# Optimization experiments

Measured on AMD Instinct MI355X. Metric: run time of the kernel, lower is better.

The kernel has to match this reference:

```python
import jax, jax.numpy as jnp
import numpy as np

EPS = 1e-5
CHUNK = 256
N_LAYERS = 4
D_MODEL = 1024
D_INNER = 2048
D_HEAD = 64
N_HEADS = 32
D_STATE = 64
D_CONV = 4
CONV_DIM = D_INNER + 2 * D_STATE  # ngroups=1
D_IN_PROJ = 2 * D_INNER + 2 * D_STATE + N_HEADS


def silu(x):
    return x * jax.nn.sigmoid(x)


def rmsnorm(x, w):
    return x * jax.lax.rsqrt(jnp.mean(x * x, axis=-1, keepdims=True) + EPS) * w


def segsum(x):
    # x: [..., T] -> [..., T, T] lower-triangular segment sums, -inf above diag
    T = x.shape[-1]
    cs = jnp.cumsum(x, axis=-1)
    ss = cs[..., :, None] - cs[..., None, :]
    mask = jnp.tril(jnp.ones((T, T), dtype=bool))
    return jnp.where(mask, ss, -jnp.inf)


def ssd(X, A, B, C, chunk):
    # X: [b,l,h,p] (already scaled by dt), A: [b,l,h] (= dt * A_head), B,C: [b,l,n] (ngroups=1)
    b, l, h, p = X.shape
    c = l // chunk
    X = X.reshape(b, c, chunk, h, p)
    A = A.reshape(b, c, chunk, h).transpose(0, 3, 1, 2)  # [b,h,c,l]
    B = B.reshape(b, c, chunk, -1)
    C = C.reshape(b, c, chunk, -1)
    Acs = jnp.cumsum(A, axis=-1)  # [b,h,c,l]
    # intra-chunk (diagonal blocks)
    Lm = jnp.exp(segsum(A))  # [b,h,c,l,l]
    Y_diag = jnp.einsum('bcln,bcsn,bhcls,bcshp->bclhp', C, B, Lm, X)
    # chunk end states
    decay_states = jnp.exp(Acs[..., -1:] - Acs)  # [b,h,c,l]
    states = jnp.einsum('bcln,bhcl,bclhp->bchpn', B, decay_states, X)
    # inter-chunk recurrence (c is small -> dense segsum over chunks)
    A_last = jnp.pad(Acs[..., -1], ((0, 0), (0, 0), (1, 0)))  # [b,h,c+1]
    decay_chunk = jnp.exp(segsum(A_last))  # [b,h,c+1,c+1]
    states = jnp.concatenate([jnp.zeros_like(states[:, :1]), states], axis=1)
    new_states = jnp.einsum('bhzc,bchpn->bzhpn', decay_chunk, states)
    states = new_states[:, :-1]  # state entering each chunk
    Y_off = jnp.einsum('bcln,bchpn,bhcl->bclhp', C, states, jnp.exp(Acs))
    return (Y_diag + Y_off).reshape(b, l, h, p)


def mamba2_layer(x, in_w, conv_w, conv_b, dt_bias, A_log, D, gnorm_w, out_w):
    b, l, _ = x.shape
    zxbcdt = jnp.einsum('bld,ed->ble', x, in_w)  # [b,l,D_IN_PROJ]
    z = zxbcdt[..., :D_INNER]
    xBC = zxbcdt[..., D_INNER:D_INNER + CONV_DIM]
    dt = zxbcdt[..., D_INNER + CONV_DIM:]  # [b,l,h]
    # depthwise causal conv1d + silu
    xpad = jnp.pad(xBC, ((0, 0), (D_CONV - 1, 0), (0, 0)))
    xconv = conv_b
    for k in range(D_CONV):
        xconv = xconv + xpad[:, k:k + l, :] * conv_w[:, k]
    xBC = silu(xconv)
    x_in = xBC[..., :D_INNER]
    B = xBC[..., D_INNER:D_INNER + D_STATE]
    C = xBC[..., D_INNER + D_STATE:]
    dt = jax.nn.softplus(dt + dt_bias)  # [b,l,h]
    A = -jnp.exp(A_log)  # [h]
    X = x_in.reshape(b, l, N_HEADS, D_HEAD)
    y = ssd(X * dt[..., None], dt * A, B, C, CHUNK)
    y = y + D[None, None, :, None] * X
    y = y.reshape(b, l, D_INNER)
    y = rmsnorm(y * silu(z), gnorm_w)
    return jnp.einsum('ble,de->bld', y, out_w)


def setup_inputs() -> dict:
    key = jax.random.key(0)
    ks = jax.random.split(key, 8)
    x = jax.random.normal(ks[0], (2, 2048, D_MODEL), dtype=jnp.float32)
    in_proj_w = jax.random.normal(ks[1], (N_LAYERS, D_IN_PROJ, D_MODEL), dtype=jnp.float32) * 0.02
    conv_w = jax.random.uniform(ks[2], (N_LAYERS, CONV_DIM, D_CONV), dtype=jnp.float32, minval=-0.5, maxval=0.5)
    conv_b = jnp.zeros((N_LAYERS, CONV_DIM), dtype=jnp.float32)
    A_log = jnp.log(jax.random.uniform(ks[3], (N_LAYERS, N_HEADS), dtype=jnp.float32, minval=1.0, maxval=16.0))
    dt0 = jax.random.uniform(ks[4], (N_LAYERS, N_HEADS), dtype=jnp.float32, minval=0.001, maxval=0.1)
    dt_bias = dt0 + jnp.log(-jnp.expm1(-dt0))  # inverse softplus
    D = jnp.ones((N_LAYERS, N_HEADS), dtype=jnp.float32)
    gnorm_w = jnp.ones((N_LAYERS, D_INNER), dtype=jnp.float32)
    out_proj_w = jax.random.normal(ks[5], (N_LAYERS, D_MODEL, D_INNER), dtype=jnp.float32) * 0.02
    rms_w = jnp.ones((N_LAYERS, D_MODEL), dtype=jnp.float32)
    return {"x": x, "in_proj_w": in_proj_w, "conv_w": conv_w, "conv_b": conv_b,
            "dt_bias": dt_bias, "A_log": A_log, "D": D, "gnorm_w": gnorm_w,
            "out_proj_w": out_proj_w, "rms_w": rms_w}


def reference(x, in_proj_w, conv_w, conv_b, dt_bias, A_log, D, gnorm_w, out_proj_w, rms_w):
    for i in range(N_LAYERS):
        x = x + mamba2_layer(rmsnorm(x, rms_w[i]), in_proj_w[i], conv_w[i], conv_b[i],
                             dt_bias[i], A_log[i], D[i], gnorm_w[i], out_proj_w[i])
    return x
```

## Files before the change

kernel.cpp:

```cpp
#include <hip/hip_runtime.h>
#include <cmath>

#define BATCH 2
#define LSEQ 2048
#define DMODEL 1024
#define DINNER 2048
#define NHEADS 32
#define DHEAD 64
#define DSTATE 64
#define DCONV 4
#define CONVDIM (DINNER + 2*DSTATE)
#define DINPROJ (2*DINNER + 2*DSTATE + NHEADS)
#define DINPROJ_PAD 4352
#define CHUNKSZ 256
#define NCHUNK (LSEQ/CHUNKSZ)
#define MROWS (BATCH*LSEQ)
#define EPSF 1e-5f

typedef __attribute__((ext_vector_type(8))) short shortx8;
typedef __attribute__((ext_vector_type(4))) short shortx4;
typedef __attribute__((ext_vector_type(4))) float floatx4;

__device__ __forceinline__ ushort f2bf(float f) {
  unsigned u = __float_as_uint(f);
  unsigned r = (u + 0x7fffu + ((u >> 16) & 1u)) >> 16;
  return (ushort)r;
}
__device__ __forceinline__ float bf2f(ushort b) {
  return __uint_as_float(((unsigned)b) << 16);
}

__device__ __forceinline__ shortx8 pack8(float4 a, float4 b) {
  shortx8 r;
  r[0] = (short)f2bf(a.x); r[1] = (short)f2bf(a.y);
  r[2] = (short)f2bf(a.z); r[3] = (short)f2bf(a.w);
  r[4] = (short)f2bf(b.x); r[5] = (short)f2bf(b.y);
  r[6] = (short)f2bf(b.z); r[7] = (short)f2bf(b.w);
  return r;
}

__device__ __forceinline__ void async_load16(const void* g, void* l) {
  __builtin_amdgcn_global_load_lds(
      (const __attribute__((address_space(1))) void*)g,
      (__attribute__((address_space(3))) void*)l, 16, 0, 0);
}

__device__ __forceinline__ float block_reduce_sum_256(float v, float* sb) {
  for (int off = 32; off > 0; off >>= 1) v += __shfl_down(v, off, 64);
  int lane = threadIdx.x & 63, wid = threadIdx.x >> 6;
  if (lane == 0) sb[wid] = v;
  __syncthreads();
  return sb[0] + sb[1] + sb[2] + sb[3];
}

__global__ __launch_bounds__(256) void cvt_bf16_k(const float* __restrict__ src,
                                                  ushort* __restrict__ dst,
                                                  size_t n_src, size_t n_dst) {
  size_t i = (size_t)blockIdx.x * 256 + threadIdx.x;
  if (i >= n_dst) return;
  float v = (i < n_src) ? src[i] : 0.f;
  dst[i] = f2bf(v);
}

__global__ __launch_bounds__(256) void rmsnorm_k(const float* __restrict__ x,
                                                 const float* __restrict__ w,
                                                 ushort* __restrict__ out) {
  __shared__ float sb[4];
  int r = blockIdx.x;
  const float* xr = x + (size_t)r * DMODEL;
  ushort* orow = out + (size_t)r * DMODEL;
  float v[4]; float ssq = 0.f;
  for (int i = 0; i < 4; i++) {
    v[i] = xr[threadIdx.x + i * 256];
    ssq += v[i] * v[i];
  }
  float s = block_reduce_sum_256(ssq, sb);
  float sc = rsqrtf(s / (float)DMODEL + EPSF);
  for (int i = 0; i < 4; i++) {
    int c = threadIdx.x + i * 256;
    orow[c] = f2bf(v[i] * sc * w[c]);
  }
}

__device__ __forceinline__ void stage_tile(const ushort* __restrict__ A,
                                           const ushort* __restrict__ B,
                                           char* lb, int m0, int n0, int K, int k0,
                                           int wid, int rA, int sA) {
#pragma unroll
  for (int rd = 0; rd < 2; rd++) {
    int r = rd * 64 + rA;
    int sl = sA ^ ((r ^ (r >> 2)) & 3);
    async_load16(A + (size_t)(m0 + r) * K + (k0 + sl * 8), lb + rd * 4096 + wid * 1024);
  }
#pragma unroll
  for (int rd = 0; rd < 2; rd++) {
    int r = rd * 64 + rA;
    int sl = sA ^ ((r ^ (r >> 2)) & 3);
    async_load16(B + (size_t)(n0 + r) * K + (k0 + sl * 8), lb + 8192 + rd * 4096 + wid * 1024);
  }
}

__global__ __launch_bounds__(256, 2) void gemm_nt_mfma_pipe(const ushort* __restrict__ A,
                                                            const ushort* __restrict__ B,
                                                            float* __restrict__ C,
                                                            ushort* __restrict__ Cbf,
                                                            const float* __restrict__ resid,
                                                            int M, int N, int K) {
  __shared__ __align__(16) char lds[4][16384];
  int tid = threadIdx.x;
  int wid = tid >> 6, lane = tid & 63;
  int quad = lane >> 4, lrow = lane & 15;
  int m0 = blockIdx.y * 128, n0 = blockIdx.x * 128;
  int wm = (wid >> 1) * 64, wn = (wid & 1) * 64;
  int rA = tid >> 2, sA = tid & 3;

  floatx4 acc[4][4];
#pragma unroll
  for (int i = 0; i < 4; i++)
#pragma unroll
    for (int j = 0; j < 4; j++) acc[i][j] = (floatx4){0.f, 0.f, 0.f, 0.f};

  int NT = K >> 5;
#pragma unroll
  for (int t = 0; t < 3; t++)
    if (t < NT) stage_tile(A, B, lds[t & 3], m0, n0, K, t * 32, wid, rA, sA);

  for (int t = 0; t < NT; t++) {
    if (t + 3 < NT) stage_tile(A, B, lds[(t + 3) & 3], m0, n0, K, (t + 3) * 32, wid, rA, sA);
    int rem = NT - 1 - t;
    if (rem >= 3)      asm volatile("s_waitcnt vmcnt(12)" ::: "memory");
    else if (rem == 2) asm volatile("s_waitcnt vmcnt(8)" ::: "memory");
    else if (rem == 1) asm volatile("s_waitcnt vmcnt(4)" ::: "memory");
    else               asm volatile("s_waitcnt vmcnt(0)" ::: "memory");
    __builtin_amdgcn_s_barrier();
    __builtin_amdgcn_sched_barrier(0);

    const char* Ab = lds[t & 3];
    const char* Bb = Ab + 8192;
    shortx8 af[4], bfr[4];
#pragma unroll
    for (int i = 0; i < 4; i++) {
      int r = wm + i * 16 + lrow;
      af[i] = *(const shortx8*)(Ab + r * 64 + ((quad ^ ((r ^ (r >> 2)) & 3)) << 4));
    }
#pragma unroll
    for (int j = 0; j < 4; j++) {
      int r = wn + j * 16 + lrow;
      bfr[j] = *(const shortx8*)(Bb + r * 64 + ((quad ^ ((r ^ (r >> 2)) & 3)) << 4));
    }
    __builtin_amdgcn_s_setprio(1);
#pragma unroll
    for (int i = 0; i < 4; i++)
#pragma unroll
      for (int j = 0; j < 4; j++)
        acc[i][j] = __builtin_amdgcn_mfma_f32_16x16x32_bf16(af[i], bfr[j], acc[i][j], 0, 0, 0);
    __builtin_amdgcn_s_setprio(0);
    __builtin_amdgcn_sched_barrier(0);
    __builtin_amdgcn_s_barrier();
    __builtin_amdgcn_sched_barrier(0);
  }

  if (Cbf) {
#pragma unroll
    for (int i = 0; i < 4; i++) {
      int r0 = m0 + wm + i * 16 + quad * 4;
#pragma unroll
      for (int j = 0; j < 4; j++) {
        int n = n0 + wn + j * 16 + lrow;
        if (n < N)
#pragma unroll
          for (int r = 0; r < 4; r++)
            Cbf[(size_t)(r0 + r) * N + n] = f2bf(acc[i][j][r]);
      }
    }
  } else {
    bool hasR = (resid != nullptr);
#pragma unroll
    for (int i = 0; i < 4; i++) {
      int r0 = m0 + wm + i * 16 + quad * 4;
#pragma unroll
      for (int j = 0; j < 4; j++) {
        int n = n0 + wn + j * 16 + lrow;
        if (n < N) {
#pragma unroll
          for (int r = 0; r < 4; r++) {
            size_t idx = (size_t)(r0 + r) * N + n;
            float v = acc[i][j][r];
            if (hasR) v += resid[idx];
            C[idx] = v;
          }
        }
      }
    }
  }
}

__global__ __launch_bounds__(256) void conv_silu_k(const ushort* __restrict__ zxbf,
                                                   const float* __restrict__ cw,
                                                   const float* __restrict__ cb,
                                                   ushort* __restrict__ xbf) {
  int ch = blockIdx.x * 256 + threadIdx.x;
  if (ch >= CONVDIM) return;
  int r = blockIdx.y;
  int b = r >> 11, l = r & (LSEQ - 1);
  float acc = cb[ch];
  for (int k = 0; k < DCONV; k++) {
    int ls = l - (DCONV - 1) + k;
    if (ls >= 0)
      acc += bf2f(zxbf[(size_t)(b * LSEQ + ls) * DINPROJ + DINNER + ch]) * cw[ch * DCONV + k];
  }
  float s = acc / (1.f + expf(-acc));
  xbf[(size_t)r * CONVDIM + ch] = f2bf(s);
}

__global__ __launch_bounds__(256) void cumsum_k(const ushort* __restrict__ zxbf,
                                                const float* __restrict__ dt_bias,
                                                const float* __restrict__ A_log,
                                                float* __restrict__ dt_sp,
                                                float* __restrict__ dtA_cs) {
  __shared__ float buf[256];
  int bid = blockIdx.x;
  int h = bid & 31, c = (bid >> 5) & 7, b = bid >> 8;
  int l = threadIdx.x;
  float Aneg = -expf(A_log[h]);
  int row = b * LSEQ + c * CHUNKSZ + l;
  float v = bf2f(zxbf[(size_t)row * DINPROJ + DINNER + CONVDIM + h]) + dt_bias[h];
  float dtv = (v > 20.f) ? v : log1pf(expf(v));
  dt_sp[row * 32 + h] = dtv;
  buf[l] = dtv * Aneg;
  __syncthreads();
  for (int off = 1; off < 256; off <<= 1) {
    float add = (l >= off) ? buf[l - off] : 0.f;
    __syncthreads();
    buf[l] += add;
    __syncthreads();
  }
  dtA_cs[(size_t)bid * CHUNKSZ + l] = buf[l];
}

#define ST_STRIDE 72
__global__ __launch_bounds__(256) void states_mfma(const ushort* __restrict__ xbf,
                                                   const float* __restrict__ dt_sp,
                                                   const float* __restrict__ dtA_cs,
                                                   float* __restrict__ st_raw) {
  __shared__ ushort XT[64 * ST_STRIDE];
  __shared__ ushort BT[64 * ST_STRIDE];
  __shared__ float wrow[64];
  int bid = blockIdx.x;
  int h = bid & 31, c = (bid >> 5) & 7, b = bid >> 8;
  int tid = threadIdx.x;
  int w = tid >> 6, lane = tid & 63;
  int quad = lane >> 4, lrow = lane & 15;
  int cbase = bid * CHUNKSZ;
  int rowbase = b * LSEQ + c * CHUNKSZ;
  float T = dtA_cs[cbase + CHUNKSZ - 1];
  floatx4 acc[4];
  for (int jt = 0; jt < 4; jt++) acc[jt] = (floatx4){0.f, 0.f, 0.f, 0.f};
  int half = tid & 31, srb = tid >> 5;
  for (int lt = 0; lt < 4; lt++) {
    __syncthreads();
    if (tid < 64) {
      int row = rowbase + lt * 64 + tid;
      wrow[tid] = dt_sp[row * 32 + h] * __expf(T - dtA_cs[cbase + lt * 64 + tid]);
    }
    __syncthreads();
    for (int pass = 0; pass < 8; pass++) {
      int sr = srb + pass * 8;
      int row = rowbase + lt * 64 + sr;
      uint bv = *(const uint*)(xbf + (size_t)row * CONVDIM + DINNER + 2 * half);
      uint xv = *(const uint*)(xbf + (size_t)row * CONVDIM + h * DHEAD + 2 * half);
      float wv = wrow[sr];
      BT[(2 * half) * ST_STRIDE + sr]     = (ushort)(bv & 0xffff);
      BT[(2 * half + 1) * ST_STRIDE + sr] = (ushort)(bv >> 16);
      XT[(2 * half) * ST_STRIDE + sr]     = f2bf(bf2f((ushort)(xv & 0xffff)) * wv);
      XT[(2 * half + 1) * ST_STRIDE + sr] = f2bf(bf2f((ushort)(xv >> 16)) * wv);
    }
    __syncthreads();
    for (int kk = 0; kk < 64; kk += 32) {
      shortx8 af = *(const shortx8*)&XT[(w * 16 + lrow) * ST_STRIDE + kk + quad * 8];
      for (int jt = 0; jt < 4; jt++) {
        shortx8 bf = *(const shortx8*)&BT[(jt * 16 + lrow) * ST_STRIDE + kk + quad * 8];
        acc[jt] = __builtin_amdgcn_mfma_f32_16x16x32_bf16(af, bf, acc[jt], 0, 0, 0);
      }
    }
  }
  size_t base = (size_t)bid * (DHEAD * DSTATE);
  for (int jt = 0; jt < 4; jt++) {
    int n = jt * 16 + lrow;
    for (int r = 0; r < 4; r++) {
      int p = w * 16 + quad * 4 + r;
      st_raw[base + (size_t)p * 64 + n] = acc[jt][r];
    }
  }
}

__global__ __launch_bounds__(256) void scan_k(float* __restrict__ st,
                                              const float* __restrict__ dtA_cs) {
  int bid = blockIdx.x;
  int h = bid & 31, b = bid >> 5;
  int tid = threadIdx.x;
  float s[16];
  for (int i = 0; i < 16; i++) s[i] = 0.f;
  for (int c = 0; c < NCHUNK; c++) {
    int g = (b * NCHUNK + c) * 32 + h;
    float dec = expf(dtA_cs[(size_t)g * CHUNKSZ + CHUNKSZ - 1]);
    size_t base = (size_t)g * (DHEAD * DSTATE);
    for (int i = 0; i < 16; i++) {
      int idx = tid + i * 256;
      float raw = st[base + idx];
      st[base + idx] = s[i];
      s[i] = s[i] * dec + raw;
    }
  }
}

#define BS_STRIDE 72
#define XT_STRIDE 68
#define PW_STRIDE 72
__global__ __launch_bounds__(256) void ydiag_mfma(const ushort* __restrict__ xbf,
                                                  const float* __restrict__ dt_sp,
                                                  const float* __restrict__ dtA_cs,
                                                  const float* __restrict__ st_in,
                                                  ushort* __restrict__ Y) {
  __shared__ ushort Bs[64 * BS_STRIDE];
  __shared__ ushort XsT[64 * XT_STRIDE];
  __shared__ ushort Pw[4 * 16 * PW_STRIDE];
  __shared__ float cs[256];
  int tid = threadIdx.x;
  int w = tid >> 6, lane = tid & 63;
  int quad = lane >> 4, lrow = lane & 15;
  int bid = blockIdx.x;
  int lt = bid & 3, h = (bid >> 2) & 31, c = (bid >> 7) & 7, b = bid >> 10;
  int g = (b * NCHUNK + c) * 32 + h;
  int cbase = g * CHUNKSZ;
  int rowbase = b * LSEQ + c * CHUNKSZ;

  cs[tid] = dtA_cs[cbase + tid];
  __syncthreads();

  int mrow = lt * 64 + w * 16;
  float csl[4];
  for (int r = 0; r < 4; r++) csl[r] = cs[mrow + quad * 4 + r];

  shortx8 Cf[2];
  {
    const ushort* cp = xbf + (size_t)(rowbase + mrow + lrow) * CONVDIM + DINNER + DSTATE;
    for (int q = 0; q < 2; q++)
      Cf[q] = *(const shortx8*)(cp + q * 32 + quad * 8);
  }

  floatx4 acc[4];
  for (int jt = 0; jt < 4; jt++) acc[jt] = (floatx4){0.f, 0.f, 0.f, 0.f};
  const float* stp = st_in + (size_t)g * (DHEAD * DSTATE);
  for (int q = 0; q < 2; q++) {
    for (int jt = 0; jt < 4; jt++) {
      const float* sp = stp + (size_t)(jt * 16 + lrow) * 64 + q * 32 + quad * 8;
      shortx8 sf = pack8(*(const float4*)sp, *(const float4*)(sp + 4));
      acc[jt] = __builtin_amdgcn_mfma_f32_16x16x32_bf16(Cf[q], sf, acc[jt], 0, 0, 0);
    }
  }
  for (int jt = 0; jt < 4; jt++)
    for (int r = 0; r < 4; r++) acc[jt][r] *= __expf(csl[r]);

  ushort* myP = Pw + w * 16 * PW_STRIDE;
  int half = tid & 31, srb = tid >> 5;
  for (int st = 0; st <= lt; st++) {
    __syncthreads();
    for (int pass = 0; pass < 8; pass++) {
      int sr = srb + pass * 8;
      int row = rowbase + st * 64 + sr;
      uint bv = *(const uint*)(xbf + (size_t)row * CONVDIM + DINNER + 2 * half);
      *(uint*)&Bs[sr * BS_STRIDE + 2 * half] = bv;
      float dtv = dt_sp[row * 32 + h];
      uint xv = *(const uint*)(xbf + (size_t)row * CONVDIM + h * DHEAD + 2 * half);
      XsT[(2 * half) * XT_STRIDE + sr]     = f2bf(bf2f((ushort)(xv & 0xffff)) * dtv);
      XsT[(2 * half + 1) * XT_STRIDE + sr] = f2bf(bf2f((ushort)(xv >> 16)) * dtv);
    }
    __syncthreads();
    for (int jt = 0; jt < 4; jt++) {
      floatx4 s = (floatx4){0.f, 0.f, 0.f, 0.f};
      for (int q = 0; q < 2; q++) {
        shortx8 bfr = *(const shortx8*)&Bs[(jt * 16 + lrow) * BS_STRIDE + q * 32 + quad * 8];
        s = __builtin_amdgcn_mfma_f32_16x16x32_bf16(Cf[q], bfr, s, 0, 0, 0);
      }
      int scol = st * 64 + jt * 16 + lrow;
      float css = cs[scol];
      for (int r = 0; r < 4; r++) {
        int l = mrow + quad * 4 + r;
        float v = (scol <= l) ? s[r] * __expf(csl[r] - css) : 0.f;
        myP[(quad * 4 + r) * PW_STRIDE + jt * 16 + lrow] = f2bf(v);
      }
    }
    shortx8 pf[2];
    for (int q = 0; q < 2; q++)
      pf[q] = *(const shortx8*)&myP[lrow * PW_STRIDE + q * 32 + quad * 8];
    for (int jt = 0; jt < 4; jt++) {
      for (int q = 0; q < 2; q++) {
        const ushort* xp = &XsT[(jt * 16 + lrow) * XT_STRIDE + q * 32 + quad * 8];
        shortx4 lo = *(const shortx4*)xp;
        shortx4 hi = *(const shortx4*)(xp + 4);
        shortx8 xf = __builtin_shufflevector(lo, hi, 0, 1, 2, 3, 4, 5, 6, 7);
        acc[jt] = __builtin_amdgcn_mfma_f32_16x16x32_bf16(pf[q], xf, acc[jt], 0, 0, 0);
      }
    }
  }
  int growb = rowbase + mrow + quad * 4;
  for (int jt = 0; jt < 4; jt++)
    for (int r = 0; r < 4; r++)
      Y[(size_t)(growb + r) * DINNER + h * DHEAD + jt * 16 + lrow] = f2bf(acc[jt][r]);
}

__global__ __launch_bounds__(256) void gatenorm_k(const ushort* __restrict__ Ybf,
                                                  const ushort* __restrict__ zxbf,
                                                  const ushort* __restrict__ xbf,
                                                  const float* __restrict__ Dvec,
                                                  const float* __restrict__ gw,
                                                  ushort* __restrict__ obf) {
  __shared__ float sb[4];
  int r = blockIdx.x;
  const ushort* yr = Ybf + (size_t)r * DINNER;
  const ushort* zr = zxbf + (size_t)r * DINPROJ;
  const ushort* xr = xbf + (size_t)r * CONVDIM;
  ushort* orow = obf + (size_t)r * DINNER;
  float t[8]; float ssq = 0.f;
  for (int i = 0; i < 8; i++) {
    int cc = threadIdx.x + i * 256;
    float z = bf2f(zr[cc]);
    float yv = bf2f(yr[cc]) + Dvec[cc >> 6] * bf2f(xr[cc]);
    float gv = yv * (z / (1.f + expf(-z)));
    t[i] = gv;
    ssq += gv * gv;
  }
  float s = block_reduce_sum_256(ssq, sb);
  float sc = rsqrtf(s / (float)DINNER + EPSF);
  for (int i = 0; i < 8; i++) {
    int cc = threadIdx.x + i * 256;
    orow[cc] = f2bf(t[i] * sc * gw[cc]);
  }
}

extern "C" void kernel_launch(void* const* d_in, const int* in_sizes, int n_in,
                              void* d_out, int out_size, void* d_ws, size_t ws_size,
                              hipStream_t stream) {
  const float* x_in     = (const float*)d_in[0];
  const float* in_w     = (const float*)d_in[1];
  const float* conv_w   = (const float*)d_in[2];
  const float* conv_b   = (const float*)d_in[3];
  const float* dt_bias  = (const float*)d_in[4];
  const float* A_log    = (const float*)d_in[5];
  const float* Dvec     = (const float*)d_in[6];
  const float* gnorm_w  = (const float*)d_in[7];
  const float* out_w    = (const float*)d_in[8];
  const float* rms_w    = (const float*)d_in[9];
  float* out = (float*)d_out;

  float* ws = (float*)d_ws;
  size_t o = 0;
  float* x_cur  = ws + o; o += (size_t)MROWS * DMODEL;
  ushort* zx_bf = (ushort*)(ws + o); o += (size_t)MROWS * DINPROJ / 2;
  ushort* xbf   = (ushort*)(ws + o); o += (size_t)MROWS * CONVDIM / 2;
  float* dt_sp  = ws + o; o += (size_t)MROWS * NHEADS;
  float* dtA_cs = ws + o; o += (size_t)BATCH * NCHUNK * NHEADS * CHUNKSZ;
  float* st     = ws + o; o += (size_t)BATCH * NCHUNK * NHEADS * DHEAD * DSTATE;
  ushort* Ybf   = (ushort*)(ws + o); o += (size_t)MROWS * DINNER / 2;
  ushort* act_bf = (ushort*)(ws + o); o += (size_t)MROWS * DINNER / 2;
  ushort* w_bf   = (ushort*)(ws + o); o += (size_t)DINPROJ_PAD * DMODEL / 2;

  hipMemcpyAsync(x_cur, x_in, (size_t)MROWS * DMODEL * sizeof(float),
                 hipMemcpyDeviceToDevice, stream);

  for (int i = 0; i < 4; i++) {
    const float* in_w_i   = in_w    + (size_t)i * DINPROJ * DMODEL;
    const float* conv_w_i = conv_w  + (size_t)i * CONVDIM * DCONV;
    const float* conv_b_i = conv_b  + (size_t)i * CONVDIM;
    const float* dtb_i    = dt_bias + (size_t)i * NHEADS;
    const float* Alog_i   = A_log   + (size_t)i * NHEADS;
    const float* D_i      = Dvec    + (size_t)i * NHEADS;
    const float* gw_i     = gnorm_w + (size_t)i * DINNER;
    const float* out_w_i  = out_w   + (size_t)i * DMODEL * DINNER;
    const float* rms_w_i  = rms_w   + (size_t)i * DMODEL;

    {
      size_t ns = (size_t)DINPROJ * DMODEL, nd = (size_t)DINPROJ_PAD * DMODEL;
      cvt_bf16_k<<<(nd + 255) / 256, 256, 0, stream>>>(in_w_i, w_bf, ns, nd);
    }
    rmsnorm_k<<<MROWS, 256, 0, stream>>>(x_cur, rms_w_i, act_bf);
    gemm_nt_mfma_pipe<<<dim3(DINPROJ_PAD / 128, MROWS / 128), 256, 0, stream>>>(
        act_bf, w_bf, nullptr, zx_bf, nullptr, MROWS, DINPROJ, DMODEL);
    conv_silu_k<<<dim3((CONVDIM + 255) / 256, MROWS), 256, 0, stream>>>(
        zx_bf, conv_w_i, conv_b_i, xbf);
    cumsum_k<<<BATCH * NCHUNK * NHEADS, 256, 0, stream>>>(zx_bf, dtb_i, Alog_i, dt_sp, dtA_cs);
    states_mfma<<<BATCH * NCHUNK * NHEADS, 256, 0, stream>>>(xbf, dt_sp, dtA_cs, st);
    scan_k<<<BATCH * NHEADS, 256, 0, stream>>>(st, dtA_cs);
    ydiag_mfma<<<BATCH * NCHUNK * NHEADS * 4, 256, 0, stream>>>(
        xbf, dt_sp, dtA_cs, st, Ybf);
    gatenorm_k<<<MROWS, 256, 0, stream>>>(Ybf, zx_bf, xbf, D_i, gw_i, act_bf);
    {
      size_t ns = (size_t)DMODEL * DINNER;
      cvt_bf16_k<<<(ns + 255) / 256, 256, 0, stream>>>(out_w_i, w_bf, ns, ns);
    }
    float* outC = (i == 3) ? out : x_cur;
    gemm_nt_mfma_pipe<<<dim3(DMODEL / 128, MROWS / 128), 256, 0, stream>>>(
        act_bf, w_bf, outC, nullptr, x_cur, MROWS, DMODEL, DINNER);
  }
}
```

Measured before the change: 1.085 ms.

## Remap GEMM blocks per XCD, five-buffer pipeline, vectorize conv, split scan

The GEMM now uses a 1D grid and remaps block IDs so that each of the 8 XCDs works on a contiguous rectangle of output tiles, which should improve L2 reuse. It also moves from a 4-slot to a 5-slot LDS ring, letting it drop the trailing barrier in each k-iteration. The depthwise conv is rewritten so each thread computes 8 channels by 8 rows from a vectorized sliding window. The state scan is split across 4 blocks per head to raise parallelism. The extra LDS (80KB per block) may reduce occupancy below the declared 2 blocks per CU.

New measurement: 988.0 us. -9.0%, faster.

```diff
diff --git a/kernel.cpp b/kernel.cpp
--- a/kernel.cpp
+++ b/kernel.cpp
@@ -105,12 +105,21 @@
                                                             float* __restrict__ C,
                                                             ushort* __restrict__ Cbf,
                                                             const float* __restrict__ resid,
-                                                            int M, int N, int K) {
-  __shared__ __align__(16) char lds[4][16384];
+                                                            int M, int N, int K,
+                                                            int nbx, int rw, int rh) {
+  __shared__ __align__(16) char lds[5][16384];
   int tid = threadIdx.x;
   int wid = tid >> 6, lane = tid & 63;
   int quad = lane >> 4, lrow = lane & 15;
-  int m0 = blockIdx.y * 128, n0 = blockIdx.x * 128;
+
+  int d = blockIdx.x;
+  int xcd = d & 7, wi = d >> 3;
+  int ra = nbx / rw;
+  int rn = xcd % ra, rm = xcd / ra;
+  int bx = rn * rw + wi % rw;
+  int by = rm * rh + wi / rw;
+
+  int m0 = by * 128, n0 = bx * 128;
   int wm = (wid >> 1) * 64, wn = (wid & 1) * 64;
   int rA = tid >> 2, sA = tid & 3;
 
@@ -123,10 +132,15 @@
   int NT = K >> 5;
 #pragma unroll
   for (int t = 0; t < 3; t++)
-    if (t < NT) stage_tile(A, B, lds[t & 3], m0, n0, K, t * 32, wid, rA, sA);
-
+    stage_tile(A, B, lds[t], m0, n0, K, t * 32, wid, rA, sA);
+
+  int cur = 0, sb = 3;
   for (int t = 0; t < NT; t++) {
-    if (t + 3 < NT) stage_tile(A, B, lds[(t + 3) & 3], m0, n0, K, (t + 3) * 32, wid, rA, sA);
+    __builtin_amdgcn_sched_barrier(0);
+    if (t + 3 < NT) {
+      stage_tile(A, B, lds[sb], m0, n0, K, (t + 3) * 32, wid, rA, sA);
+      sb = (sb == 4) ? 0 : sb + 1;
+    }
     int rem = NT - 1 - t;
     if (rem >= 3)      asm volatile("s_waitcnt vmcnt(12)" ::: "memory");
     else if (rem == 2) asm volatile("s_waitcnt vmcnt(8)" ::: "memory");
@@ -135,8 +149,9 @@
     __builtin_amdgcn_s_barrier();
     __builtin_amdgcn_sched_barrier(0);
 
-    const char* Ab = lds[t & 3];
+    const char* Ab = lds[cur];
     const char* Bb = Ab + 8192;
+    cur = (cur == 4) ? 0 : cur + 1;
     shortx8 af[4], bfr[4];
 #pragma unroll
     for (int i = 0; i < 4; i++) {
@@ -155,9 +170,6 @@
       for (int j = 0; j < 4; j++)
         acc[i][j] = __builtin_amdgcn_mfma_f32_16x16x32_bf16(af[i], bfr[j], acc[i][j], 0, 0, 0);
     __builtin_amdgcn_s_setprio(0);
-    __builtin_amdgcn_sched_barrier(0);
-    __builtin_amdgcn_s_barrier();
-    __builtin_amdgcn_sched_barrier(0);
   }
 
   if (Cbf) {
@@ -195,22 +207,52 @@
   }
 }
 
-__global__ __launch_bounds__(256) void conv_silu_k(const ushort* __restrict__ zxbf,
-                                                   const float* __restrict__ cw,
-                                                   const float* __restrict__ cb,
-                                                   ushort* __restrict__ xbf) {
-  int ch = blockIdx.x * 256 + threadIdx.x;
-  if (ch >= CONVDIM) return;
-  int r = blockIdx.y;
-  int b = r >> 11, l = r & (LSEQ - 1);
-  float acc = cb[ch];
-  for (int k = 0; k < DCONV; k++) {
-    int ls = l - (DCONV - 1) + k;
-    if (ls >= 0)
-      acc += bf2f(zxbf[(size_t)(b * LSEQ + ls) * DINPROJ + DINNER + ch]) * cw[ch * DCONV + k];
-  }
-  float s = acc / (1.f + expf(-acc));
-  xbf[(size_t)r * CONVDIM + ch] = f2bf(s);
+__global__ __launch_bounds__(256) void conv_silu_v2(const ushort* __restrict__ zxbf,
+                                                    const float* __restrict__ cw,
+                                                    const float* __restrict__ cb,
+                                                    ushort* __restrict__ xbf) {
+  int r0 = blockIdx.x * 8;
+  int bstart = r0 & ~(LSEQ - 1);
+  int tid = threadIdx.x;
+#pragma unroll
+  for (int rep = 0; rep < 2; rep++) {
+    int ch;
+    if (rep == 0) ch = tid * 8;
+    else { if (tid >= (CONVDIM - 2048) / 8) break; ch = 2048 + tid * 8; }
+    float wv[8][4], bias[8];
+#pragma unroll
+    for (int j = 0; j < 8; j++) {
+      float4 w4 = *(const float4*)(cw + (ch + j) * 4);
+      wv[j][0] = w4.x; wv[j][1] = w4.y; wv[j][2] = w4.z; wv[j][3] = w4.w;
+      bias[j] = cb[ch + j];
+    }
+    float xw[11][8];
+#pragma unroll
+    for (int wr = 0; wr < 11; wr++) {
+      int rr = r0 - 3 + wr;
+      if (rr < bstart) {
+#pragma unroll
+        for (int j = 0; j < 8; j++) xw[wr][j] = 0.f;
+      } else {
+        shortx8 v = *(const shortx8*)(zxbf + (size_t)rr * DINPROJ + DINNER + ch);
+#pragma unroll
+        for (int j = 0; j < 8; j++) xw[wr][j] = bf2f((ushort)v[j]);
+      }
+    }
+#pragma unroll
+    for (int o = 0; o < 8; o++) {
+      shortx8 ov;
+#pragma unroll
+      for (int j = 0; j < 8; j++) {
+        float acc = bias[j];
+#pragma unroll
+        for (int k = 0; k < 4; k++) acc += xw[o + k][j] * wv[j][k];
+        float s = acc / (1.f + expf(-acc));
+        ov[j] = (short)f2bf(s);
+      }
+      *(shortx8*)(xbf + (size_t)(r0 + o) * CONVDIM + ch) = ov;
+    }
+  }
 }
 
 __global__ __launch_bounds__(256) void cumsum_k(const ushort* __restrict__ zxbf,
@@ -297,15 +339,16 @@
 __global__ __launch_bounds__(256) void scan_k(float* __restrict__ st,
                                               const float* __restrict__ dtA_cs) {
   int bid = blockIdx.x;
-  int h = bid & 31, b = bid >> 5;
+  int seg = bid & 3, h = (bid >> 2) & 31, b = bid >> 7;
   int tid = threadIdx.x;
-  float s[16];
-  for (int i = 0; i < 16; i++) s[i] = 0.f;
+  int off = seg * 1024;
+  float s[4];
+  for (int i = 0; i < 4; i++) s[i] = 0.f;
   for (int c = 0; c < NCHUNK; c++) {
     int g = (b * NCHUNK + c) * 32 + h;
     float dec = expf(dtA_cs[(size_t)g * CHUNKSZ + CHUNKSZ - 1]);
-    size_t base = (size_t)g * (DHEAD * DSTATE);
-    for (int i = 0; i < 16; i++) {
+    size_t base = (size_t)g * (DHEAD * DSTATE) + off;
+    for (int i = 0; i < 4; i++) {
       int idx = tid + i * 256;
       float raw = st[base + idx];
       st[base + idx] = s[i];
@@ -485,13 +528,13 @@
       cvt_bf16_k<<<(nd + 255) / 256, 256, 0, stream>>>(in_w_i, w_bf, ns, nd);
     }
     rmsnorm_k<<<MROWS, 256, 0, stream>>>(x_cur, rms_w_i, act_bf);
-    gemm_nt_mfma_pipe<<<dim3(DINPROJ_PAD / 128, MROWS / 128), 256, 0, stream>>>(
-        act_bf, w_bf, nullptr, zx_bf, nullptr, MROWS, DINPROJ, DMODEL);
-    conv_silu_k<<<dim3((CONVDIM + 255) / 256, MROWS), 256, 0, stream>>>(
-        zx_bf, conv_w_i, conv_b_i, xbf);
+    gemm_nt_mfma_pipe<<<(DINPROJ_PAD / 128) * (MROWS / 128), 256, 0, stream>>>(
+        act_bf, w_bf, nullptr, zx_bf, nullptr, MROWS, DINPROJ, DMODEL,
+        DINPROJ_PAD / 128, 17, 8);
+    conv_silu_v2<<<MROWS / 8, 256, 0, stream>>>(zx_bf, conv_w_i, conv_b_i, xbf);
     cumsum_k<<<BATCH * NCHUNK * NHEADS, 256, 0, stream>>>(zx_bf, dtb_i, Alog_i, dt_sp, dtA_cs);
     states_mfma<<<BATCH * NCHUNK * NHEADS, 256, 0, stream>>>(xbf, dt_sp, dtA_cs, st);
-    scan_k<<<BATCH * NHEADS, 256, 0, stream>>>(st, dtA_cs);
+    scan_k<<<BATCH * NHEADS * 4, 256, 0, stream>>>(st, dtA_cs);
     ydiag_mfma<<<BATCH * NCHUNK * NHEADS * 4, 256, 0, stream>>>(
         xbf, dt_sp, dtA_cs, st, Ybf);
     gatenorm_k<<<MROWS, 256, 0, stream>>>(Ybf, zx_bf, xbf, D_i, gw_i, act_bf);
@@ -500,7 +543,8 @@
       cvt_bf16_k<<<(ns + 255) / 256, 256, 0, stream>>>(out_w_i, w_bf, ns, ns);
     }
     float* outC = (i == 3) ? out : x_cur;
-    gemm_nt_mfma_pipe<<<dim3(DMODEL / 128, MROWS / 128), 256, 0, stream>>>(
-        act_bf, w_bf, outC, nullptr, x_cur, MROWS, DMODEL, DINNER);
-  }
-}
+    gemm_nt_mfma_pipe<<<(DMODEL / 128) * (MROWS / 128), 256, 0, stream>>>(
+        act_bf, w_bf, outC, nullptr, x_cur, MROWS, DMODEL, DINNER,
+        DMODEL / 128, 4, 8);
+  }
+}
```
